# Performance work log

Hardware: AMD Instinct MI355X
Metric: run time of the kernel (lower is better)

Reference implementation:

```python
import jax, jax.numpy as jnp
import numpy as np

WIN = 9
PAD = WIN // 2    # floor(9/2) = 4
WIN_SIZE = WIN * WIN
EPS = 1e-05


def _box_sum(x):
    # 9x9 ones-kernel conv, stride 1, pad 4 (SAME size), NCHW with C=1
    filt = jnp.ones((1, 1, WIN, WIN), dtype=x.dtype)
    return jax.lax.conv_general_dilated(
        x, filt, window_strides=(1, 1),
        padding=[(PAD, PAD), (PAD, PAD)],
        dimension_numbers=('NCHW', 'OIHW', 'NCHW'))


def setup_inputs() -> dict:
    key = jax.random.key(0)
    k1, k2 = jax.random.split(key)
    I = jax.random.normal(k1, (8, 1, 1024, 1024), dtype=jnp.float32)
    J = jax.random.normal(k2, (8, 1, 1024, 1024), dtype=jnp.float32)
    return {"I": I, "J": J}


def reference(I, J):
    I_sum = _box_sum(I)
    J_sum = _box_sum(J)
    I2_sum = _box_sum(I * I)
    J2_sum = _box_sum(J * J)
    IJ_sum = _box_sum(I * J)

    u_I = I_sum / WIN_SIZE
    u_J = J_sum / WIN_SIZE

    cross = IJ_sum - u_J * I_sum - u_I * J_sum + u_I * u_J * WIN_SIZE
    I_var = I2_sum - 2 * u_I * I_sum + u_I * u_I * WIN_SIZE
    J_var = J2_sum - 2 * u_J * J_sum + u_J * u_J * WIN_SIZE

    cc = cross * cross / (I_var * J_var + EPS)
    return jnp.mean(cc)
```

## Files before the change

### kernel.cpp

```cpp
#include <hip/hip_runtime.h>

#define H 1024
#define W 1024
#define NIMG 8
#define CPT 4
#define TH 4
#define NBX 4
#define WPB 4
#define NBY (H / (TH * WPB))
#define NBLK (NBX * NBY * NIMG)
#define NWAVES (NBLK * WPB)
#define EPS 1e-5f

struct RS { float I[CPT], J[CPT], II[CPT], JJ[CPT], IJ[CPT]; };

__device__ __forceinline__ void row_rs(const float* __restrict__ Irow,
                                       const float* __restrict__ Jrow,
                                       int X, bool okL, bool okR, RS& o) {
  float a[12], b[12];
  { float4 q = *reinterpret_cast<const float4*>(Irow + X);
    a[4]=q.x; a[5]=q.y; a[6]=q.z; a[7]=q.w;
    float4 p = *reinterpret_cast<const float4*>(Jrow + X);
    b[4]=p.x; b[5]=p.y; b[6]=p.z; b[7]=p.w; }
  if (okL) {
    float4 q = *reinterpret_cast<const float4*>(Irow + X - 4);
    a[0]=q.x; a[1]=q.y; a[2]=q.z; a[3]=q.w;
    float4 p = *reinterpret_cast<const float4*>(Jrow + X - 4);
    b[0]=p.x; b[1]=p.y; b[2]=p.z; b[3]=p.w;
  } else { a[0]=a[1]=a[2]=a[3]=0.f; b[0]=b[1]=b[2]=b[3]=0.f; }
  if (okR) {
    float4 q = *reinterpret_cast<const float4*>(Irow + X + 4);
    a[8]=q.x; a[9]=q.y; a[10]=q.z; a[11]=q.w;
    float4 p = *reinterpret_cast<const float4*>(Jrow + X + 4);
    b[8]=p.x; b[9]=p.y; b[10]=p.z; b[11]=p.w;
  } else { a[8]=a[9]=a[10]=a[11]=0.f; b[8]=b[9]=b[10]=b[11]=0.f; }

  float sI=0.f, sJ=0.f, sII=0.f, sJJ=0.f, sIJ=0.f;
  #pragma unroll
  for (int k = 0; k < 9; ++k) {
    sI += a[k]; sJ += b[k];
    sII = fmaf(a[k], a[k], sII);
    sJJ = fmaf(b[k], b[k], sJJ);
    sIJ = fmaf(a[k], b[k], sIJ);
  }
  o.I[0]=sI; o.J[0]=sJ; o.II[0]=sII; o.JJ[0]=sJJ; o.IJ[0]=sIJ;
  #pragma unroll
  for (int i = 1; i < CPT; ++i) {
    float an=a[i+8], al=a[i-1], bn=b[i+8], bl=b[i-1];
    sI += an - al;  sJ += bn - bl;
    sII = fmaf(-al, al, fmaf(an, an, sII));
    sJJ = fmaf(-bl, bl, fmaf(bn, bn, sJJ));
    sIJ = fmaf(-al, bl, fmaf(an, bn, sIJ));
    o.I[i]=sI; o.J[i]=sJ; o.II[i]=sII; o.JJ[i]=sJJ; o.IJ[i]=sIJ;
  }
}

__global__ __launch_bounds__(256, 4)
void ncc_main(const float* __restrict__ I, const float* __restrict__ J,
              float* __restrict__ partial) {
  const int tid  = threadIdx.x;
  const int lane = tid & 63, wv = tid >> 6;
  const int bid  = (int)blockIdx.x;
  const int tile = ((bid & 7) << 8) | (bid >> 3);
  const int bx   = tile & (NBX - 1);
  const int rest = tile >> 2;
  const int by   = rest & (NBY - 1);
  const int bz   = rest >> 6;
  const int X  = bx * 256 + lane * CPT;
  const int y0 = (by * WPB + wv) * TH;
  const bool okL = (X >= 4);
  const bool okR = (X + 8 <= W);
  const size_t img_off = (size_t)bz * H * W;
  const float* Ip = I + img_off;
  const float* Jp = J + img_off;

  float wI[CPT], wJ[CPT], wII[CPT], wJJ[CPT], wIJ[CPT];
  #pragma unroll
  for (int i = 0; i < CPT; ++i) { wI[i]=wJ[i]=wII[i]=wJJ[i]=wIJ[i]=0.f; }
  float acc = 0.f;
  const float inv81 = 1.0f / 81.0f;

  auto apply = [&](int r, float sgn) {
    if ((unsigned)r < (unsigned)H) {
      RS o;
      row_rs(Ip + (size_t)r * W, Jp + (size_t)r * W, X, okL, okR, o);
      #pragma unroll
      for (int i = 0; i < CPT; ++i) {
        wI[i]  = fmaf(sgn, o.I[i],  wI[i]);
        wJ[i]  = fmaf(sgn, o.J[i],  wJ[i]);
        wII[i] = fmaf(sgn, o.II[i], wII[i]);
        wJJ[i] = fmaf(sgn, o.JJ[i], wJJ[i]);
        wIJ[i] = fmaf(sgn, o.IJ[i], wIJ[i]);
      }
    }
  };
  auto emit = [&]() {
    #pragma unroll
    for (int i = 0; i < CPT; ++i) {
      float cross = fmaf(-(wI[i] * wJ[i]), inv81, wIJ[i]);
      float Iv    = fmaf(-(wI[i] * wI[i]), inv81, wII[i]);
      float Jv    = fmaf(-(wJ[i] * wJ[i]), inv81, wJJ[i]);
      acc = fmaf(cross * cross,
                 __builtin_amdgcn_rcpf(fmaf(Iv, Jv, EPS)), acc);
    }
  };

  for (int k = 0; k < 8; ++k) apply(y0 - 4 + k, 1.0f);
  apply(y0 + 4, 1.0f);
  emit();
  for (int k = 0; k < TH - 1; ++k) {
    apply(y0 + 5 + k, 1.0f);
    apply(y0 - 4 + k, -1.0f);
    emit();
  }

  #pragma unroll
  for (int off = 32; off > 0; off >>= 1)
    acc += __shfl_down(acc, off, 64);
  if (lane == 0)
    partial[tile * WPB + wv] = acc;
}

__global__ __launch_bounds__(256)
void ncc_reduce(const float* __restrict__ partial, float* __restrict__ out) {
  __shared__ float red[4];
  const int tid = threadIdx.x;
  const float4* p4 = reinterpret_cast<const float4*>(partial);
  float s = 0.f;
  #pragma unroll
  for (int i = tid; i < NWAVES / 4; i += 256) {
    float4 v = p4[i];
    s += (v.x + v.y) + (v.z + v.w);
  }
  #pragma unroll
  for (int off = 32; off > 0; off >>= 1)
    s += __shfl_down(s, off, 64);
  if ((tid & 63) == 0) red[tid >> 6] = s;
  __syncthreads();
  if (tid == 0)
    out[0] = (red[0] + red[1] + red[2] + red[3]) *
             (1.0f / (float)((size_t)NIMG * H * W));
}

extern "C" void kernel_launch(void* const* d_in, const int* in_sizes, int n_in,
                              void* d_out, int out_size, void* d_ws, size_t ws_size,
                              hipStream_t stream) {
  const float* I = (const float*)d_in[0];
  const float* J = (const float*)d_in[1];
  float* out     = (float*)d_out;
  float* partial = (float*)d_ws;

  hipLaunchKernelGGL(ncc_main, dim3(NBLK), dim3(256), 0, stream, I, J, partial);
  hipLaunchKernelGGL(ncc_reduce, dim3(1), dim3(256), 0, stream, partial, out);
}
```

Baseline: 121.2 us.

## Widen per-thread column tile to 8 to cut redundant halo loads

Each thread now computes 8 output columns instead of 4, loading 16 floats per row (one more float4 per image) rather than 12, so less of each load is spent on halo columns. Blocks per image drop accordingly, with the tile index mapping and bounds checks adjusted. The per-row accumulation is folded directly into the window registers instead of going through an intermediate struct. It raises register pressure and halves the number of blocks, which may reduce occupancy and parallelism.

```diff
diff --git a/kernel.cpp b/kernel.cpp
--- a/kernel.cpp
+++ b/kernel.cpp
@@ -3,25 +3,32 @@
 #define H 1024
 #define W 1024
 #define NIMG 8
-#define CPT 4
+#define CPT 8
 #define TH 4
-#define NBX 4
+#define NBX 2
 #define WPB 4
 #define NBY (H / (TH * WPB))
 #define NBLK (NBX * NBY * NIMG)
 #define NWAVES (NBLK * WPB)
 #define EPS 1e-5f
 
-struct RS { float I[CPT], J[CPT], II[CPT], JJ[CPT], IJ[CPT]; };
-
-__device__ __forceinline__ void row_rs(const float* __restrict__ Irow,
-                                       const float* __restrict__ Jrow,
-                                       int X, bool okL, bool okR, RS& o) {
-  float a[12], b[12];
-  { float4 q = *reinterpret_cast<const float4*>(Irow + X);
-    a[4]=q.x; a[5]=q.y; a[6]=q.z; a[7]=q.w;
-    float4 p = *reinterpret_cast<const float4*>(Jrow + X);
-    b[4]=p.x; b[5]=p.y; b[6]=p.z; b[7]=p.w; }
+__device__ __forceinline__ void rs_apply(
+    const float* __restrict__ Ip, const float* __restrict__ Jp,
+    int r, int X, bool okL, bool okR, float scale,
+    float wI[CPT], float wJ[CPT], float wII[CPT], float wJJ[CPT],
+    float wIJ[CPT])
+{
+  const float* Irow = Ip + (size_t)r * W;
+  const float* Jrow = Jp + (size_t)r * W;
+  float a[16], b[16];
+  { float4 q0 = *reinterpret_cast<const float4*>(Irow + X);
+    float4 q1 = *reinterpret_cast<const float4*>(Irow + X + 4);
+    a[4]=q0.x; a[5]=q0.y; a[6]=q0.z; a[7]=q0.w;
+    a[8]=q1.x; a[9]=q1.y; a[10]=q1.z; a[11]=q1.w;
+    float4 p0 = *reinterpret_cast<const float4*>(Jrow + X);
+    float4 p1 = *reinterpret_cast<const float4*>(Jrow + X + 4);
+    b[4]=p0.x; b[5]=p0.y; b[6]=p0.z; b[7]=p0.w;
+    b[8]=p1.x; b[9]=p1.y; b[10]=p1.z; b[11]=p1.w; }
   if (okL) {
     float4 q = *reinterpret_cast<const float4*>(Irow + X - 4);
     a[0]=q.x; a[1]=q.y; a[2]=q.z; a[3]=q.w;
@@ -29,11 +36,11 @@
     b[0]=p.x; b[1]=p.y; b[2]=p.z; b[3]=p.w;
   } else { a[0]=a[1]=a[2]=a[3]=0.f; b[0]=b[1]=b[2]=b[3]=0.f; }
   if (okR) {
-    float4 q = *reinterpret_cast<const float4*>(Irow + X + 4);
-    a[8]=q.x; a[9]=q.y; a[10]=q.z; a[11]=q.w;
-    float4 p = *reinterpret_cast<const float4*>(Jrow + X + 4);
-    b[8]=p.x; b[9]=p.y; b[10]=p.z; b[11]=p.w;
-  } else { a[8]=a[9]=a[10]=a[11]=0.f; b[8]=b[9]=b[10]=b[11]=0.f; }
+    float4 q = *reinterpret_cast<const float4*>(Irow + X + 8);
+    a[12]=q.x; a[13]=q.y; a[14]=q.z; a[15]=q.w;
+    float4 p = *reinterpret_cast<const float4*>(Jrow + X + 8);
+    b[12]=p.x; b[13]=p.y; b[14]=p.z; b[15]=p.w;
+  } else { a[12]=a[13]=a[14]=a[15]=0.f; b[12]=b[13]=b[14]=b[15]=0.f; }
 
   float sI=0.f, sJ=0.f, sII=0.f, sJJ=0.f, sIJ=0.f;
   #pragma unroll
@@ -43,7 +50,11 @@
     sJJ = fmaf(b[k], b[k], sJJ);
     sIJ = fmaf(a[k], b[k], sIJ);
   }
-  o.I[0]=sI; o.J[0]=sJ; o.II[0]=sII; o.JJ[0]=sJJ; o.IJ[0]=sIJ;
+  wI[0]  = fmaf(scale, sI,  wI[0]);
+  wJ[0]  = fmaf(scale, sJ,  wJ[0]);
+  wII[0] = fmaf(scale, sII, wII[0]);
+  wJJ[0] = fmaf(scale, sJJ, wJJ[0]);
+  wIJ[0] = fmaf(scale, sIJ, wIJ[0]);
   #pragma unroll
   for (int i = 1; i < CPT; ++i) {
     float an=a[i+8], al=a[i-1], bn=b[i+8], bl=b[i-1];
@@ -51,7 +62,11 @@
     sII = fmaf(-al, al, fmaf(an, an, sII));
     sJJ = fmaf(-bl, bl, fmaf(bn, bn, sJJ));
     sIJ = fmaf(-al, bl, fmaf(an, bn, sIJ));
-    o.I[i]=sI; o.J[i]=sJ; o.II[i]=sII; o.JJ[i]=sJJ; o.IJ[i]=sIJ;
+    wI[i]  = fmaf(scale, sI,  wI[i]);
+    wJ[i]  = fmaf(scale, sJ,  wJ[i]);
+    wII[i] = fmaf(scale, sII, wII[i]);
+    wJJ[i] = fmaf(scale, sJJ, wJJ[i]);
+    wIJ[i] = fmaf(scale, sIJ, wIJ[i]);
   }
 }
 
@@ -61,15 +76,15 @@
   const int tid  = threadIdx.x;
   const int lane = tid & 63, wv = tid >> 6;
   const int bid  = (int)blockIdx.x;
-  const int tile = ((bid & 7) << 8) | (bid >> 3);
+  const int tile = ((bid & 7) << 7) | (bid >> 3);
   const int bx   = tile & (NBX - 1);
-  const int rest = tile >> 2;
+  const int rest = tile >> 1;
   const int by   = rest & (NBY - 1);
   const int bz   = rest >> 6;
-  const int X  = bx * 256 + lane * CPT;
+  const int X  = bx * 512 + lane * CPT;
   const int y0 = (by * WPB + wv) * TH;
   const bool okL = (X >= 4);
-  const bool okR = (X + 8 <= W);
+  const bool okR = (X + 12 <= W);
   const size_t img_off = (size_t)bz * H * W;
   const float* Ip = I + img_off;
   const float* Jp = J + img_off;
@@ -81,18 +96,8 @@
   const float inv81 = 1.0f / 81.0f;
 
   auto apply = [&](int r, float sgn) {
-    if ((unsigned)r < (unsigned)H) {
-      RS o;
-      row_rs(Ip + (size_t)r * W, Jp + (size_t)r * W, X, okL, okR, o);
-      #pragma unroll
-      for (int i = 0; i < CPT; ++i) {
-        wI[i]  = fmaf(sgn, o.I[i],  wI[i]);
-        wJ[i]  = fmaf(sgn, o.J[i],  wJ[i]);
-        wII[i] = fmaf(sgn, o.II[i], wII[i]);
-        wJJ[i] = fmaf(sgn, o.JJ[i], wJJ[i]);
-        wIJ[i] = fmaf(sgn, o.IJ[i], wIJ[i]);
-      }
-    }
+    if ((unsigned)r < (unsigned)H)
+      rs_apply(Ip, Jp, r, X, okL, okR, sgn, wI, wJ, wII, wJJ, wIJ);
   };
   auto emit = [&]() {
     #pragma unroll
```

New measurement: 122.0 us. Within noise of the previous version (+0.6%).
